# Kernel optimization log

Hardware: AMD Instinct MI355X
Metric: run time of the kernel (lower is better)

## Reference

```python
import jax, jax.numpy as jnp
import numpy as np
from jax import lax

B, A, ACT, ID, FEAT, HID, NA = 4096, 20, 21, 20, 32, 64, 21
VIEW = 5 * 7 * 6  # 210
NB = A * (1 + ACT)  # 440


def setup_inputs() -> dict:
    key = jax.random.key(0)
    ks = jax.random.split(key, 16)
    view = jax.random.normal(ks[0], (B, VIEW), dtype=jnp.float32)
    feat = jax.random.normal(ks[1], (B, FEAT), dtype=jnp.float32)
    # neighbor ids in [-2, ID): -2 => absent (skipped), -1 => self, >=0 => neighbor index
    ids = jax.random.randint(ks[2], (B, A), -2, ID).astype(jnp.float32)
    act_idx = jax.random.randint(ks[3], (B, A), 0, ACT)
    acts = jax.nn.one_hot(act_idx, ACT, dtype=jnp.float32)
    zero_act = jax.random.uniform(ks[4], (B, A)) < 0.3
    acts = jnp.where(zero_act[..., None], 0.0, acts)
    nb = jnp.concatenate([ids[..., None], acts], axis=-1).reshape(B, NB)
    obs = jnp.concatenate([view, feat, nb], axis=1)  # [B, 682]
    s = 0.05
    return {
        'obs': obs,
        'conv1_w': jax.random.normal(ks[5], (32, 5, 3, 3), jnp.float32) * s,
        'conv1_b': jax.random.normal(ks[6], (32,), jnp.float32) * s,
        'conv2_w': jax.random.normal(ks[7], (32, 32, 3, 3), jnp.float32) * s,
        'conv2_b': jax.random.normal(ks[8], (32,), jnp.float32) * s,
        'fc1_w': jax.random.normal(ks[9], (192, HID), jnp.float32) * s,
        'fc1_b': jax.random.normal(ks[10], (HID,), jnp.float32) * s,
        'fc2_w': jax.random.normal(ks[11], (HID + FEAT + ID + ACT, HID), jnp.float32) * s,
        'fc2_b': jax.random.normal(ks[12], (HID,), jnp.float32) * s,
        'fc3_w': jax.random.normal(ks[13], (HID, NA), jnp.float32) * s,
        'fc3_b': jax.random.normal(ks[14], (NA,), jnp.float32) * s,
    }


def reference(obs, conv1_w, conv1_b, conv2_w, conv2_b, fc1_w, fc1_b, fc2_w, fc2_b, fc3_w, fc3_b):
    view = obs[:, :VIEW].reshape(-1, 5, 7, 6)
    feat = obs[:, VIEW:VIEW + FEAT]
    nb = obs[:, -NB:].reshape(-1, A, 1 + ACT)
    ids = nb[..., 0]          # [B, A] float ids
    acts = nb[..., 1:]        # [B, A, ACT]

    dn = ('NCHW', 'OIHW', 'NCHW')
    o = jax.nn.relu(lax.conv_general_dilated(view, conv1_w, (1, 1), 'VALID', dimension_numbers=dn)
                    + conv1_b[None, :, None, None])
    o = jax.nn.relu(lax.conv_general_dilated(o, conv2_w, (1, 1), 'VALID', dimension_numbers=dn)
                    + conv2_b[None, :, None, None])          # [B, 32, 3, 2]
    x = jax.nn.relu(o.reshape(-1, 192) @ fc1_w + fc1_b)      # [B, HID]

    # fc2 is linear in the concat(x, feat, id_onehot, act); split its weight accordingly.
    W2x = fc2_w[:HID]
    W2f = fc2_w[HID:HID + FEAT]
    W2id = fc2_w[HID + FEAT:HID + FEAT + ID]
    W2act = fc2_w[HID + FEAT + ID:]

    id_int = ids.astype(jnp.int32)
    # self (id==-1) uses zeros for the id one-hot; one_hot gives zeros for negatives.
    idvec = jax.nn.one_hot(id_int, ID, dtype=obs.dtype)       # [B, A, ID]

    base = x @ W2x + feat @ W2f + fc2_b                        # [B, HID]
    idterm = jnp.einsum('bai,ih->bah', idvec, W2id)            # [B, A, HID]
    actterm = jnp.einsum('baj,jh->bah', acts, W2act)           # [B, A, HID]

    # single-row case (self or known neighbor action)
    h_s = jax.nn.relu(base[:, None, :] + idterm + actterm)     # [B, A, HID]
    q_s = h_s @ fc3_w + fc3_b                                  # [B, A, NA]

    # expand case: unknown action => enumerate all ACT one-hot actions and sum q
    h_e = jax.nn.relu(base[:, None, None, :] + idterm[:, :, None, :] + W2act[None, None, :, :])  # [B, A, ACT, HID]
    q_e = (h_e @ fc3_w + fc3_b).sum(axis=2)                    # [B, A, NA]

    valid = id_int >= -1
    act_zero = jnp.all(acts == 0.0, axis=-1)
    expand = valid & (id_int >= 0) & act_zero

    q_agent = jnp.where(expand[..., None], q_e, q_s)
    q_agent = jnp.where(valid[..., None], q_agent, 0.0)
    return q_agent.sum(axis=1)                                 # [B, NA]
```

## Files before the change

### kernel.cpp

```cpp
#include <hip/hip_runtime.h>

typedef __attribute__((ext_vector_type(8))) short bf16x8;
typedef __attribute__((ext_vector_type(4))) float f32x4;

constexpr int OBS  = 682;
constexpr int ACTN = 21;
constexpr int MB   = 8;

constexpr int WS_C1U  = 0;
constexpr int WS_C2U  = 2048;
constexpr int WS_F1U  = 11264;
constexpr int WS_TOTU = 23552;

__device__ __forceinline__ unsigned short f2bf(float x) {
    unsigned u = __float_as_uint(x);
    return (unsigned short)((u + 0x7FFFu + ((u >> 16) & 1u)) >> 16);
}

__global__ void repack_b(const float* __restrict__ c1w, const float* __restrict__ c2w,
                         const float* __restrict__ f1w, unsigned short* __restrict__ wsu) {
    int i = blockIdx.x * 256 + threadIdx.x;
    if (i >= WS_TOTU) return;
    int frag = i >> 9, within = i & 511;
    int l = within >> 3, j = within & 7;
    int q = l >> 4, l15 = l & 15;
    float v = 0.f;
    if (frag < 4) {
        int s = frag >> 1, nt = frag & 1;
        int k = 32 * s + 8 * q + j, n = 16 * nt + l15;
        if (k < 45) v = c1w[n * 45 + k];
    } else if (frag < 22) {
        int f = frag - 4, s = f >> 1, nt = f & 1;
        int k = 32 * s + 8 * q + j, n = 16 * nt + l15;
        v = c2w[n * 288 + k];
    } else {
        int f = frag - 22, s = f >> 2, nt = f & 3;
        int k = 32 * s + 8 * q + j, n = 16 * nt + l15;
        v = f1w[k * 64 + n];
    }
    wsu[i] = f2bf(v);
}

constexpr int SC1S = 648;

__global__ __launch_bounds__(512, 6) void mfma_k(
    const float* __restrict__ obs,
    const float* __restrict__ c1b, const float* __restrict__ c2b,
    const float* __restrict__ f1b, const float* __restrict__ f2w,
    const float* __restrict__ f2b, const float* __restrict__ f3w,
    const float* __restrict__ f3b,
    const unsigned short* __restrict__ wsu,
    float* __restrict__ out)
{
    const int t = threadIdx.x;
    const int w = t >> 6, l = t & 63;
    const int q = l >> 4, l15 = l & 15;
    const int b8 = blockIdx.x * MB;

    __shared__ __align__(16) unsigned short sv[MB * 280];
    __shared__ __align__(16) unsigned short sc1[MB * SC1S];
    __shared__ __align__(16) unsigned short sc2[MB * 200];
    __shared__ __align__(16) float sfeat32[MB * 32];
    __shared__ __align__(16) float sx32[MB * 64];
    __shared__ __align__(16) float sW[2624];
    __shared__ __align__(16) float sbias[224];
    __shared__ int smeta[MB * 20];
    __shared__ __align__(16) unsigned short tap1[48];
    __shared__ __align__(16) unsigned short tap2[288];

    float* sh32 = sx32;

    for (int e = t; e < MB * 210; e += 512) {
        int row = e / 210, i2 = e - row * 210;
        int c = i2 / 42, rem = i2 - c * 42;
        int r3 = rem / 6, col = rem - r3 * 6;
        sv[row * 280 + c * 56 + r3 * 8 + col] = f2bf(obs[(long)(b8 + row) * OBS + i2]);
    }
    if (t < MB * 32) {
        int row = t >> 5, j = t & 31;
        sfeat32[t] = obs[(long)(b8 + row) * OBS + 210 + j];
    }
    {
        const float4* srcw = (const float4*)(f2w + 96 * 64);
        float4* dw = (float4*)sW;
        if (t < 512) { dw[t] = srcw[t]; if (t < 144) dw[512 + t] = srcw[512 + t]; }
    }
    if (t < 224) {
        float v = 0.f;
        if (t < 32) v = c1b[t];
        else if (t < 64) v = c2b[t - 32];
        else if (t < 128) v = f1b[t - 64];
        else if (t < 192) v = f2b[t - 128];
        else if (t < 213) v = f3b[t - 192];
        sbias[t] = v;
    }
    if (t < 48) {
        int c = t / 9, rem = t - c * 9;
        tap1[t] = (t < 45) ? (unsigned short)(c * 56 + (rem / 3) * 8 + (rem % 3))
                           : (unsigned short)0;
    }
    if (t < 288) {
        int ic = t / 9, rem = t - ic * 9;
        tap2[t] = (unsigned short)(ic * 20 + (rem / 3) * 4 + (rem % 3));
    }
    if (t < MB * 20) {
        int row = t / 20, a = t - row * 20;
        const float* nb = obs + (long)(b8 + row) * OBS + 242 + a * 22;
        int id = (int)nb[0];
        int js = -1;
        #pragma unroll
        for (int j = 0; j < ACTN; ++j) {
            float av = nb[1 + j];
            js = (av != 0.f && js < 0) ? j : js;
        }
        int mode = (id < -1) ? 0 : ((id >= 0 && js < 0) ? 1 : 2);
        smeta[t] = ((id + 2) << 8) | (mode << 5) | (js + 1);
    }
    __syncthreads();

    {
        #pragma unroll
        for (int u = 0; u < 3; ++u) {
            int p = w + 8 * u;
            if (p < 20) {
                int mt = p >> 1, nt = p & 1;
                int m = mt * 16 + l15;
                int brow = m / 20, pos = m - brow * 20;
                int base1 = brow * 280 + ((pos >> 2) << 3) + (pos & 3);
                f32x4 acc = {0.f, 0.f, 0.f, 0.f};
                {
                    const unsigned short* tp = &tap1[8 * q];
                    bf16x8 a;
                    #pragma unroll
                    for (int j = 0; j < 8; ++j)
                        a[j] = (short)sv[base1 + tp[j]];
                    bf16x8 bb = *(const bf16x8*)&wsu[WS_C1U + (0 + nt) * 512 + l * 8];
                    acc = __builtin_amdgcn_mfma_f32_16x16x32_bf16(a, bb, acc, 0, 0, 0);
                }
                {
                    bf16x8 a = {0, 0, 0, 0, 0, 0, 0, 0};
                    if (q < 2) {
                        const unsigned short* tp = &tap1[32 + 8 * q];
                        #pragma unroll
                        for (int j = 0; j < 8; ++j) {
                            unsigned short v = sv[base1 + tp[j]];
                            a[j] = (8 * q + j < 13) ? (short)v : (short)0;
                        }
                    }
                    bf16x8 bb = *(const bf16x8*)&wsu[WS_C1U + (2 + nt) * 512 + l * 8];
                    acc = __builtin_amdgcn_mfma_f32_16x16x32_bf16(a, bb, acc, 0, 0, 0);
                }
                int oc = nt * 16 + l15;
                float bias = sbias[oc];
                #pragma unroll
                for (int r = 0; r < 4; ++r) {
                    int mm = mt * 16 + 4 * q + r;
                    int row = mm / 20, ps = mm - row * 20;
                    sc1[row * SC1S + oc * 20 + ps] = f2bf(fmaxf(acc[r] + bias, 0.f));
                }
            }
        }
    }
    __syncthreads();

    if (w < 6) {
        int mt = w >> 1, nt = w & 1;
        int m = mt * 16 + l15;
        int rowm = m / 6, posm = m - rowm * 6;
        int base2 = rowm * SC1S + ((posm >> 1) << 2) + (posm & 1);
        f32x4 acc = {0.f, 0.f, 0.f, 0.f};
        #pragma unroll
        for (int s = 0; s < 9; ++s) {
            const unsigned short* tp = &tap2[32 * s + 8 * q];
            bf16x8 a;
            #pragma unroll
            for (int j = 0; j < 8; ++j)
                a[j] = (short)sc1[base2 + tp[j]];
            bf16x8 bb = *(const bf16x8*)&wsu[WS_C2U + (s * 2 + nt) * 512 + l * 8];
            acc = __builtin_amdgcn_mfma_f32_16x16x32_bf16(a, bb, acc, 0, 0, 0);
        }
        int oc = nt * 16 + l15;
        float bias = sbias[32 + oc];
        #pragma unroll
        for (int r = 0; r < 4; ++r) {
            int mm = mt * 16 + 4 * q + r;
            int row = mm / 6, ps = mm - row * 6;
            sc2[row * 200 + oc * 6 + ps] = f2bf(fmaxf(acc[r] + bias, 0.f));
        }
    }
    __syncthreads();

    if (w < 4) {
        int nt = w;
        f32x4 acc = {0.f, 0.f, 0.f, 0.f};
        #pragma unroll
        for (int s = 0; s < 6; ++s) {
            bf16x8 a = *(const bf16x8*)&sc2[l15 * 200 + 32 * s + 8 * q];
            bf16x8 bb = *(const bf16x8*)&wsu[WS_F1U + (s * 4 + nt) * 512 + l * 8];
            acc = __builtin_amdgcn_mfma_f32_16x16x32_bf16(a, bb, acc, 0, 0, 0);
        }
        int h = nt * 16 + l15;
        float bias = sbias[64 + h];
        #pragma unroll
        for (int r = 0; r < 4; ++r) {
            int row = 4 * q + r;
            if (row < MB) sx32[row * 64 + h] = fmaxf(acc[r] + bias, 0.f);
        }
    }
    __syncthreads();

    float cnt;
    {
        const int row = w;
        float a0 = sbias[128 + l], a1 = 0.f;
        #pragma unroll 4
        for (int k = 0; k < 64; k += 2) {
            a0 = fmaf(sx32[row * 64 + k],     f2w[(k    ) * 64 + l], a0);
            a1 = fmaf(sx32[row * 64 + k + 1], f2w[(k + 1) * 64 + l], a1);
        }
        #pragma unroll 4
        for (int k = 0; k < 32; k += 2) {
            a0 = fmaf(sfeat32[row * 32 + k],     f2w[(64 + k    ) * 64 + l], a0);
            a1 = fmaf(sfeat32[row * 32 + k + 1], f2w[(64 + k + 1) * 64 + l], a1);
        }
        const float base_l = a0 + a1;
        float hacc = 0.f;
        cnt = 0.f;
        for (int a = 0; a < 20; ++a) {
            int m = smeta[row * 20 + a];
            int mode = (m >> 5) & 3;
            if (mode == 0) continue;
            int id = (m >> 8) - 2;
            int js = (m & 31) - 1;
            float u = base_l + ((id >= 0) ? sW[id * 64 + l] : 0.f);
            if (mode == 1) {
                float h0 = 0.f, h1 = 0.f, h2 = 0.f;
                #pragma unroll
                for (int j = 0; j < ACTN; j += 3) {
                    h0 += fmaxf(u + sW[1280 + (j    ) * 64 + l], 0.f);
                    h1 += fmaxf(u + sW[1280 + (j + 1) * 64 + l], 0.f);
                    h2 += fmaxf(u + sW[1280 + (j + 2) * 64 + l], 0.f);
                }
                hacc += (h0 + h1) + h2;
                cnt  += 21.f;
            } else {
                float ar = (js >= 0) ? sW[1280 + js * 64 + l] : 0.f;
                hacc += fmaxf(u + ar, 0.f);
                cnt  += 1.f;
            }
        }
        sh32[row * 64 + l] = hacc;
    }

    if (l < ACTN) {
        float qv = cnt * sbias[192 + l];
        float q1 = 0.f;
        #pragma unroll 4
        for (int h = 0; h < 64; h += 2) {
            qv = fmaf(sh32[w * 64 + h],     f3w[(h    ) * 21 + l], qv);
            q1 = fmaf(sh32[w * 64 + h + 1], f3w[(h + 1) * 21 + l], q1);
        }
        out[(long)(b8 + w) * 21 + l] = qv + q1;
    }
}

__device__ __forceinline__ float comp4(float4 v, int i) {
    return (i == 0) ? v.x : (i == 1) ? v.y : (i == 2) ? v.z : v.w;
}

constexpr int S_V = 0, S_OBS = 280, S_C1 = 968, S_PART = 1608, S_C2 = 1992,
              S_X = 2184, S_H = 2248, S_TOT = 2312;

__global__ __launch_bounds__(64, 4) void fallback_k(
    const float* __restrict__ obs,
    const float* __restrict__ c1w, const float* __restrict__ c1b,
    const float* __restrict__ c2w, const float* __restrict__ c2b,
    const float* __restrict__ f1w, const float* __restrict__ f1b,
    const float* __restrict__ f2w, const float* __restrict__ f2b,
    const float* __restrict__ f3w, const float* __restrict__ f3b,
    float* __restrict__ out)
{
    const int b = blockIdx.x, t = threadIdx.x;
    __shared__ __align__(16) float sb[S_TOT];
    __shared__ int s_meta[20];
    {
        const float* orow = obs + (long)b * OBS;
        #pragma unroll
        for (int k = 0; k < 4; ++k) {
            int i = t + k * 64;
            if (i < 210) {
                int c = i / 42, rem = i - 42 * c, r = rem / 6, col = rem - 6 * r;
                sb[S_V + c * 56 + r * 8 + col] = orow[i];
            }
        }
        #pragma unroll
        for (int k = 0; k < 8; ++k) {
            int i = 210 + t + k * 64;
            if (i < OBS) sb[S_OBS + i] = orow[i];
        }
    }
    __syncthreads();
    if (t < 20) {
        const float* nb = &sb[S_OBS + 242 + t * 22];
        int id = (int)nb[0], js = -1;
        #pragma unroll
        for (int j = 0; j < ACTN; ++j) {
            float av = nb[1 + j];
            js = (av != 0.f && js < 0) ? j : js;
        }
        int mode = (id < -1) ? 0 : ((id >= 0 && js < 0) ? 1 : 2);
        s_meta[t] = ((id + 2) << 8) | (mode << 5) | (js + 1);
    }
    {
        const int oc = t & 31, s = t >> 5;
        float acc[12];
        #pragma unroll
        for (int i = 0; i < 12; ++i) acc[i] = 0.f;
        #pragma unroll
        for (int c = 0; c < 5; ++c) {
            float wv[9];
            #pragma unroll
            for (int k = 0; k < 9; ++k) wv[k] = c1w[oc * 45 + c * 9 + k];
            #pragma unroll
            for (int rr = 0; rr < 5; ++rr) {
                const float* rowp = &sb[S_V + c * 56 + (2 * s + rr) * 8];
                float4 v0 = *(const float4*)rowp;
                float2 v1 = *(const float2*)(rowp + 4);
                float c0 = v0.x, c1 = v0.y, c2 = v0.z, c3 = v0.w, c4 = v1.x, c5 = v1.y;
                #pragma unroll
                for (int kh = 0; kh < 3; ++kh) {
                    int ohl = rr - kh;
                    if (ohl < 0 || ohl > 2) continue;
                    acc[ohl*4+0] = fmaf(c0, wv[kh*3+0], acc[ohl*4+0]);
                    acc[ohl*4+0] = fmaf(c1, wv[kh*3+1], acc[ohl*4+0]);
                    acc[ohl*4+0] = fmaf(c2, wv[kh*3+2], acc[ohl*4+0]);
                    acc[ohl*4+1] = fmaf(c1, wv[kh*3+0], acc[ohl*4+1]);
                    acc[ohl*4+1] = fmaf(c2, wv[kh*3+1], acc[ohl*4+1]);
                    acc[ohl*4+1] = fmaf(c3, wv[kh*3+2], acc[ohl*4+1]);
                    acc[ohl*4+2] = fmaf(c2, wv[kh*3+0], acc[ohl*4+2]);
                    acc[ohl*4+2] = fmaf(c3, wv[kh*3+1], acc[ohl*4+2]);
                    acc[ohl*4+2] = fmaf(c4, wv[kh*3+2], acc[ohl*4+2]);
                    acc[ohl*4+3] = fmaf(c3, wv[kh*3+0], acc[ohl*4+3]);
                    acc[ohl*4+3] = fmaf(c4, wv[kh*3+1], acc[ohl*4+3]);
                    acc[ohl*4+3] = fmaf(c5, wv[kh*3+2], acc[ohl*4+3]);
                }
            }
        }
        float bias = c1b[oc];
        #pragma unroll
        for (int ohl = 0; ohl < 3; ++ohl) {
            int oh = 2 * s + ohl;
            float4 o4 = make_float4(fmaxf(acc[ohl*4+0] + bias, 0.f), fmaxf(acc[ohl*4+1] + bias, 0.f),
                                    fmaxf(acc[ohl*4+2] + bias, 0.f), fmaxf(acc[ohl*4+3] + bias, 0.f));
            *(float4*)&sb[S_C1 + oc * 20 + oh * 4] = o4;
        }
    }
    __syncthreads();
    {
        const int oc = t & 31, half = t >> 5;
        float a0=0,a1=0,a2=0,a3=0,a4=0,a5=0;
        #pragma unroll 4
        for (int icc = 0; icc < 16; ++icc) {
            const int ic = half * 16 + icc;
            const float4* rp = (const float4*)&sb[S_C1 + ic * 20];
            float4 r0 = rp[0], r1 = rp[1], r2 = rp[2], r3 = rp[3], r4 = rp[4];
            float wv[9];
            #pragma unroll
            for (int k = 0; k < 9; ++k) wv[k] = c2w[oc * 288 + ic * 9 + k];
            #pragma unroll
            for (int kh = 0; kh < 3; ++kh) {
                float4 ra = (kh == 0) ? r0 : (kh == 1) ? r1 : r2;
                float4 rb = (kh == 0) ? r1 : (kh == 1) ? r2 : r3;
                float4 rc = (kh == 0) ? r2 : (kh == 1) ? r3 : r4;
                #pragma unroll
                for (int kw = 0; kw < 3; ++kw) {
                    float ww = wv[kh * 3 + kw];
                    a0 = fmaf(comp4(ra, kw),     ww, a0);
                    a1 = fmaf(comp4(ra, kw + 1), ww, a1);
                    a2 = fmaf(comp4(rb, kw),     ww, a2);
                    a3 = fmaf(comp4(rb, kw + 1), ww, a3);
                    a4 = fmaf(comp4(rc, kw),     ww, a4);
                    a5 = fmaf(comp4(rc, kw + 1), ww, a5);
                }
            }
        }
        float* pp = &sb[S_PART + (half * 32 + oc) * 6];
        pp[0]=a0; pp[1]=a1; pp[2]=a2; pp[3]=a3; pp[4]=a4; pp[5]=a5;
    }
    __syncthreads();
    if (t < 32) {
        float bias = c2b[t];
        #pragma unroll
        for (int p = 0; p < 6; ++p)
            sb[S_C2 + t * 6 + p] = fmaxf(sb[S_PART + t * 6 + p] + sb[S_PART + (32 + t) * 6 + p] + bias, 0.f);
    }
    __syncthreads();
    {
        float a0 = f1b[t], a1 = 0.f;
        const float4* xp = (const float4*)&sb[S_C2];
        #pragma unroll 4
        for (int kq = 0; kq < 48; ++kq) {
            float4 x = xp[kq];
            a0 = fmaf(x.x, f1w[(4*kq+0)*64+t], a0);
            a1 = fmaf(x.y, f1w[(4*kq+1)*64+t], a1);
            a0 = fmaf(x.z, f1w[(4*kq+2)*64+t], a0);
            a1 = fmaf(x.w, f1w[(4*kq+3)*64+t], a1);
        }
        sb[S_X + t] = fmaxf(a0 + a1, 0.f);
    }
    __syncthreads();
    float base_t;
    {
        float a0 = f2b[t], a1 = 0.f;
        const float4* xp = (const float4*)&sb[S_X];
        #pragma unroll 4
        for (int kq = 0; kq < 16; ++kq) {
            float4 x = xp[kq];
            a0 = fmaf(x.x, f2w[(4*kq+0)*64+t], a0);
            a1 = fmaf(x.y, f2w[(4*kq+1)*64+t], a1);
            a0 = fmaf(x.z, f2w[(4*kq+2)*64+t], a0);
            a1 = fmaf(x.w, f2w[(4*kq+3)*64+t], a1);
        }
        const float2* fp = (const float2*)&sb[S_OBS + 210];
        #pragma unroll 4
        for (int i2 = 0; i2 < 16; ++i2) {
            float2 v = fp[i2];
            a0 = fmaf(v.x, f2w[(64 + i2*2+0)*64+t], a0);
            a1 = fmaf(v.y, f2w[(64 + i2*2+1)*64+t], a1);
        }
        base_t = a0 + a1;
    }
    const float* W2id = f2w + 96 * 64;
    const float* W2act = f2w + 116 * 64;
    float hacc = 0.f, cnt = 0.f;
    for (int a = 0; a < 20; ++a) {
        int m = s_meta[a];
        int mode = (m >> 5) & 3;
        if (mode == 0) continue;
        int id = (m >> 8) - 2, js = (m & 31) - 1;
        float u = base_t + ((id >= 0) ? W2id[id * 64 + t] : 0.f);
        if (mode == 1) {
            float h0=0,h1=0,h2=0;
            #pragma unroll
            for (int j = 0; j < ACTN; j += 3) {
                h0 += fmaxf(u + W2act[(j    )*64+t], 0.f);
                h1 += fmaxf(u + W2act[(j + 1)*64+t], 0.f);
                h2 += fmaxf(u + W2act[(j + 2)*64+t], 0.f);
            }
            hacc += (h0 + h1) + h2; cnt += 21.f;
        } else {
            float ar = (js >= 0) ? W2act[js * 64 + t] : 0.f;
            hacc += fmaxf(u + ar, 0.f); cnt += 1.f;
        }
    }
    sb[S_H + t] = hacc;
    __syncthreads();
    if (t < ACTN) {
        float q0 = cnt * f3b[t], q1 = 0.f;
        const float4* hp = (const float4*)&sb[S_H];
        #pragma unroll 4
        for (int h4 = 0; h4 < 16; ++h4) {
            float4 v = hp[h4];
            q0 = fmaf(v.x, f3w[(h4*4+0)*21+t], q0);
            q1 = fmaf(v.y, f3w[(h4*4+1)*21+t], q1);
            q0 = fmaf(v.z, f3w[(h4*4+2)*21+t], q0);
            q1 = fmaf(v.w, f3w[(h4*4+3)*21+t], q1);
        }
        out[b * 21 + t] = q0 + q1;
    }
}

extern "C" void kernel_launch(void* const* d_in, const int* in_sizes, int n_in,
                              void* d_out, int out_size, void* d_ws, size_t ws_size,
                              hipStream_t stream) {
    const float* obs = (const float*)d_in[0];
    const float* c1w = (const float*)d_in[1];
    const float* c1b = (const float*)d_in[2];
    const float* c2w = (const float*)d_in[3];
    const float* c2b = (const float*)d_in[4];
    const float* f1w = (const float*)d_in[5];
    const float* f1b = (const float*)d_in[6];
    const float* f2w = (const float*)d_in[7];
    const float* f2b = (const float*)d_in[8];
    const float* f3w = (const float*)d_in[9];
    const float* f3b = (const float*)d_in[10];
    float* o = (float*)d_out;
    const int B = in_sizes[0] / OBS;

    if (ws_size >= (size_t)WS_TOTU * 2 && (B % MB) == 0) {
        unsigned short* wsu = (unsigned short*)d_ws;
        repack_b<<<(WS_TOTU + 255) / 256, 256, 0, stream>>>(c1w, c2w, f1w, wsu);
        mfma_k<<<B / MB, 512, 0, stream>>>(obs, c1b, c2b, f1b, f2w, f2b, f3w, f3b, wsu, o);
    } else {
        fallback_k<<<B, 64, 0, stream>>>(obs, c1w, c1b, c2w, c2b, f1w, f1b,
                                         f2w, f2b, f3w, f3b, o);
    }
}
```

Baseline: 26.97 us.

## Shrink mfma_k blocks to 256 threads and redistribute work across four waves

Reduces the fused MFMA kernel from 8 waves to 4 waves per block. Each wave now handles more conv1/conv2 tiles and two batch rows in the fc2/fc3 stage, and the shared-memory staging loops were rewritten for the smaller thread count. The intent is to cut idle waves in stages that previously used only 4–6 of 8 waves, and to allow more blocks per CU. The cost is longer serial work per wave and less latency hiding within a block.

New measurement: 33.15 us. +22.9%, slower.

```diff
diff --git a/kernel.cpp b/kernel.cpp
--- a/kernel.cpp
+++ b/kernel.cpp
@@ -43,7 +43,7 @@
 
 constexpr int SC1S = 648;
 
-__global__ __launch_bounds__(512, 6) void mfma_k(
+__global__ __launch_bounds__(256, 4) void mfma_k(
     const float* __restrict__ obs,
     const float* __restrict__ c1b, const float* __restrict__ c2b,
     const float* __restrict__ f1b, const float* __restrict__ f2w,
@@ -70,20 +70,24 @@
 
     float* sh32 = sx32;
 
-    for (int e = t; e < MB * 210; e += 512) {
+    for (int e = t; e < MB * 210; e += 256) {
         int row = e / 210, i2 = e - row * 210;
         int c = i2 / 42, rem = i2 - c * 42;
         int r3 = rem / 6, col = rem - r3 * 6;
         sv[row * 280 + c * 56 + r3 * 8 + col] = f2bf(obs[(long)(b8 + row) * OBS + i2]);
     }
-    if (t < MB * 32) {
+    {
         int row = t >> 5, j = t & 31;
-        sfeat32[t] = obs[(long)(b8 + row) * OBS + 210 + j];
+        sfeat32[row * 32 + j] = obs[(long)(b8 + row) * OBS + 210 + j];
     }
     {
         const float4* srcw = (const float4*)(f2w + 96 * 64);
         float4* dw = (float4*)sW;
-        if (t < 512) { dw[t] = srcw[t]; if (t < 144) dw[512 + t] = srcw[512 + t]; }
+        #pragma unroll
+        for (int kk = 0; kk < 3; ++kk) {
+            int i = t + kk * 256;
+            if (i < 656) dw[i] = srcw[i];
+        }
     }
     if (t < 224) {
         float v = 0.f;
@@ -99,9 +103,17 @@
         tap1[t] = (t < 45) ? (unsigned short)(c * 56 + (rem / 3) * 8 + (rem % 3))
                            : (unsigned short)0;
     }
-    if (t < 288) {
-        int ic = t / 9, rem = t - ic * 9;
-        tap2[t] = (unsigned short)(ic * 20 + (rem / 3) * 4 + (rem % 3));
+    {
+        int e = t;
+        if (e < 288) {
+            int ic = e / 9, rem = e - ic * 9;
+            tap2[e] = (unsigned short)(ic * 20 + (rem / 3) * 4 + (rem % 3));
+        }
+        e = t + 256;
+        if (e < 288) {
+            int ic = e / 9, rem = e - ic * 9;
+            tap2[e] = (unsigned short)(ic * 20 + (rem / 3) * 4 + (rem % 3));
+        }
     }
     if (t < MB * 20) {
         int row = t / 20, a = t - row * 20;
@@ -120,77 +132,81 @@
 
     {
         #pragma unroll
-        for (int u = 0; u < 3; ++u) {
-            int p = w + 8 * u;
-            if (p < 20) {
+        for (int u = 0; u < 5; ++u) {
+            int p = w + 4 * u;
+            int mt = p >> 1, nt = p & 1;
+            int m = mt * 16 + l15;
+            int brow = m / 20, pos = m - brow * 20;
+            int base1 = brow * 280 + ((pos >> 2) << 3) + (pos & 3);
+            f32x4 acc = {0.f, 0.f, 0.f, 0.f};
+            {
+                const unsigned short* tp = &tap1[8 * q];
+                bf16x8 a;
+                #pragma unroll
+                for (int j = 0; j < 8; ++j)
+                    a[j] = (short)sv[base1 + tp[j]];
+                bf16x8 bb = *(const bf16x8*)&wsu[WS_C1U + (0 + nt) * 512 + l * 8];
+                acc = __builtin_amdgcn_mfma_f32_16x16x32_bf16(a, bb, acc, 0, 0, 0);
+            }
+            {
+                bf16x8 a = {0, 0, 0, 0, 0, 0, 0, 0};
+                if (q < 2) {
+                    const unsigned short* tp = &tap1[32 + 8 * q];
+                    #pragma unroll
+                    for (int j = 0; j < 8; ++j) {
+                        unsigned short v = sv[base1 + tp[j]];
+                        a[j] = (8 * q + j < 13) ? (short)v : (short)0;
+                    }
+                }
+                bf16x8 bb = *(const bf16x8*)&wsu[WS_C1U + (2 + nt) * 512 + l * 8];
+                acc = __builtin_amdgcn_mfma_f32_16x16x32_bf16(a, bb, acc, 0, 0, 0);
+            }
+            int oc = nt * 16 + l15;
+            float bias = sbias[oc];
+            #pragma unroll
+            for (int r = 0; r < 4; ++r) {
+                int mm = mt * 16 + 4 * q + r;
+                int row = mm / 20, ps = mm - row * 20;
+                sc1[row * SC1S + oc * 20 + ps] = f2bf(fmaxf(acc[r] + bias, 0.f));
+            }
+        }
+    }
+    __syncthreads();
+
+    {
+        #pragma unroll
+        for (int u = 0; u < 2; ++u) {
+            int p = w + 4 * u;
+            if (p < 6) {
                 int mt = p >> 1, nt = p & 1;
                 int m = mt * 16 + l15;
-                int brow = m / 20, pos = m - brow * 20;
-                int base1 = brow * 280 + ((pos >> 2) << 3) + (pos & 3);
+                int rowm = m / 6, posm = m - rowm * 6;
+                int base2 = rowm * SC1S + ((posm >> 1) << 2) + (posm & 1);
                 f32x4 acc = {0.f, 0.f, 0.f, 0.f};
-                {
-                    const unsigned short* tp = &tap1[8 * q];
+                #pragma unroll
+                for (int s = 0; s < 9; ++s) {
+                    const unsigned short* tp = &tap2[32 * s + 8 * q];
                     bf16x8 a;
                     #pragma unroll
                     for (int j = 0; j < 8; ++j)
-                        a[j] = (short)sv[base1 + tp[j]];
-                    bf16x8 bb = *(const bf16x8*)&wsu[WS_C1U + (0 + nt) * 512 + l * 8];
-                    acc = __builtin_amdgcn_mfma_f32_16x16x32_bf16(a, bb, acc, 0, 0, 0);
-                }
-                {
-                    bf16x8 a = {0, 0, 0, 0, 0, 0, 0, 0};
-                    if (q < 2) {
-                        const unsigned short* tp = &tap1[32 + 8 * q];
-                        #pragma unroll
-                        for (int j = 0; j < 8; ++j) {
-                            unsigned short v = sv[base1 + tp[j]];
-                            a[j] = (8 * q + j < 13) ? (short)v : (short)0;
-                        }
-                    }
-                    bf16x8 bb = *(const bf16x8*)&wsu[WS_C1U + (2 + nt) * 512 + l * 8];
+                        a[j] = (short)sc1[base2 + tp[j]];
+                    bf16x8 bb = *(const bf16x8*)&wsu[WS_C2U + (s * 2 + nt) * 512 + l * 8];
                     acc = __builtin_amdgcn_mfma_f32_16x16x32_bf16(a, bb, acc, 0, 0, 0);
                 }
                 int oc = nt * 16 + l15;
-                float bias = sbias[oc];
+                float bias = sbias[32 + oc];
                 #pragma unroll
                 for (int r = 0; r < 4; ++r) {
                     int mm = mt * 16 + 4 * q + r;
-                    int row = mm / 20, ps = mm - row * 20;
-                    sc1[row * SC1S + oc * 20 + ps] = f2bf(fmaxf(acc[r] + bias, 0.f));
+                    int row = mm / 6, ps = mm - row * 6;
+                    sc2[row * 200 + oc * 6 + ps] = f2bf(fmaxf(acc[r] + bias, 0.f));
                 }
             }
         }
     }
     __syncthreads();
 
-    if (w < 6) {
-        int mt = w >> 1, nt = w & 1;
-        int m = mt * 16 + l15;
-        int rowm = m / 6, posm = m - rowm * 6;
-        int base2 = rowm * SC1S + ((posm >> 1) << 2) + (posm & 1);
-        f32x4 acc = {0.f, 0.f, 0.f, 0.f};
-        #pragma unroll
-        for (int s = 0; s < 9; ++s) {
-            const unsigned short* tp = &tap2[32 * s + 8 * q];
-            bf16x8 a;
-            #pragma unroll
-            for (int j = 0; j < 8; ++j)
-                a[j] = (short)sc1[base2 + tp[j]];
-            bf16x8 bb = *(const bf16x8*)&wsu[WS_C2U + (s * 2 + nt) * 512 + l * 8];
-            acc = __builtin_amdgcn_mfma_f32_16x16x32_bf16(a, bb, acc, 0, 0, 0);
-        }
-        int oc = nt * 16 + l15;
-        float bias = sbias[32 + oc];
-        #pragma unroll
-        for (int r = 0; r < 4; ++r) {
-            int mm = mt * 16 + 4 * q + r;
-            int row = mm / 6, ps = mm - row * 6;
-            sc2[row * 200 + oc * 6 + ps] = f2bf(fmaxf(acc[r] + bias, 0.f));
-        }
-    }
-    __syncthreads();
-
-    if (w < 4) {
+    {
         int nt = w;
         f32x4 acc = {0.f, 0.f, 0.f, 0.f};
         #pragma unroll
@@ -209,9 +225,10 @@
     }
     __syncthreads();
 
-    float cnt;
-    {
-        const int row = w;
+    float cnts[2];
+    #pragma unroll
+    for (int rr = 0; rr < 2; ++rr) {
+        const int row = w + 4 * rr;
         float a0 = sbias[128 + l], a1 = 0.f;
         #pragma unroll 4
         for (int k = 0; k < 64; k += 2) {
@@ -224,8 +241,7 @@
             a1 = fmaf(sfeat32[row * 32 + k + 1], f2w[(64 + k + 1) * 64 + l], a1);
         }
         const float base_l = a0 + a1;
-        float hacc = 0.f;
-        cnt = 0.f;
+        float hacc = 0.f, cnt = 0.f;
         for (int a = 0; a < 20; ++a) {
             int m = smeta[row * 20 + a];
             int mode = (m >> 5) & 3;
@@ -250,17 +266,22 @@
             }
         }
         sh32[row * 64 + l] = hacc;
+        cnts[rr] = cnt;
     }
 
     if (l < ACTN) {
-        float qv = cnt * sbias[192 + l];
-        float q1 = 0.f;
-        #pragma unroll 4
-        for (int h = 0; h < 64; h += 2) {
-            qv = fmaf(sh32[w * 64 + h],     f3w[(h    ) * 21 + l], qv);
-            q1 = fmaf(sh32[w * 64 + h + 1], f3w[(h + 1) * 21 + l], q1);
-        }
-        out[(long)(b8 + w) * 21 + l] = qv + q1;
+        #pragma unroll
+        for (int rr = 0; rr < 2; ++rr) {
+            const int row = w + 4 * rr;
+            float qv = cnts[rr] * sbias[192 + l];
+            float q1 = 0.f;
+            #pragma unroll 4
+            for (int h = 0; h < 64; h += 2) {
+                qv = fmaf(sh32[row * 64 + h],     f3w[(h    ) * 21 + l], qv);
+                q1 = fmaf(sh32[row * 64 + h + 1], f3w[(h + 1) * 21 + l], q1);
+            }
+            out[(long)(b8 + row) * 21 + l] = qv + q1;
+        }
     }
 }
 
@@ -490,7 +511,7 @@
     if (ws_size >= (size_t)WS_TOTU * 2 && (B % MB) == 0) {
         unsigned short* wsu = (unsigned short*)d_ws;
         repack_b<<<(WS_TOTU + 255) / 256, 256, 0, stream>>>(c1w, c2w, f1w, wsu);
-        mfma_k<<<B / MB, 512, 0, stream>>>(obs, c1b, c2b, f1b, f2w, f2b, f3w, f3b, wsu, o);
+        mfma_k<<<B / MB, 256, 0, stream>>>(obs, c1b, c2b, f1b, f2w, f2b, f3w, f3b, wsu, o);
     } else {
         fallback_k<<<B, 64, 0, stream>>>(obs, c1w, c1b, c2w, c2b, f1w, f1b,
                                          f2w, f2b, f3w, f3b, o);
```
